# Performance work log

Hardware: AMD Instinct MI355X
Metric: run time of the kernel (lower is better)

Reference implementation:

```python
import jax, jax.numpy as jnp
import numpy as np

B, L, C, K = 32, 8192, 32, 5  # batch, positions, channels(=filters), kernel_size
F = C  # residual add requires filters == input channels
BN_EPS = 1e-3      # keras BatchNormalization default epsilon
LEAKY_ALPHA = 0.3  # keras LeakyReLU default alpha


def setup_inputs() -> dict:
    key = jax.random.key(0)
    ks = jax.random.split(key, 4)
    # RandomUniform(-limit, limit) with limit = sqrt(2*3 / (2*K*F**2))
    limit = float(np.sqrt(2.0 * 3.0 / (2.0 * K * F * F)))
    return {
        "x": jax.random.normal(ks[0], (B, L, C), dtype=jnp.float32),
        # LocallyConnected 1: K unshared kernels [L, C, F], bias [L, F]
        "k1": jax.random.uniform(ks[1], (K, L, C, F), minval=-limit, maxval=limit, dtype=jnp.float32),
        "b1": jnp.zeros((L, F), dtype=jnp.float32),
        "gamma1": jnp.ones((F,), dtype=jnp.float32),
        "beta1": jnp.zeros((F,), dtype=jnp.float32),
        "mean1": jnp.zeros((F,), dtype=jnp.float32),
        "var1": jnp.ones((F,), dtype=jnp.float32),
        # LocallyConnected 2
        "k2": jax.random.uniform(ks[2], (K, L, F, F), minval=-limit, maxval=limit, dtype=jnp.float32),
        "b2": jnp.zeros((L, F), dtype=jnp.float32),
        "gamma2": jnp.ones((F,), dtype=jnp.float32),
        "beta2": jnp.zeros((F,), dtype=jnp.float32),
        "mean2": jnp.zeros((F,), dtype=jnp.float32),
        "var2": jnp.ones((F,), dtype=jnp.float32),
    }


def _locally_connected(x, kernels, bias):
    # x: [B, L, Cin]; kernels: [K, L, Cin, F]; bias: [L, F]
    # Original adds bias once inside the accumulator and once at the end -> 2*bias.
    out = 2.0 * bias
    for i in range(kernels.shape[0]):
        step = (i // 2) * (-1 if (i % 2 == 1) else 1)  # 0, 0, 1, -1, 2, -2, ...
        xs = jnp.roll(x, step, axis=1) if step != 0 else x
        out = out + jnp.einsum('blc,lcf->blf', xs, kernels[i])
    return out


def _bn(x, gamma, beta, mean, var):
    return gamma * (x - mean) * jax.lax.rsqrt(var + BN_EPS) + beta


def _leaky(x):
    return jnp.where(x >= 0, x, LEAKY_ALPHA * x)


def reference(x, k1, b1, gamma1, beta1, mean1, var1,
              k2, b2, gamma2, beta2, mean2, var2):
    h = _locally_connected(x, k1, b1)
    h = _bn(h, gamma1, beta1, mean1, var1)
    h = _leaky(h)
    h = _locally_connected(h, k2, b2)
    h = _bn(h, gamma2, beta2, mean2, var2)
    return _leaky(h + x)
```

## Files before the change

### kernel.cpp

```cpp
#include <hip/hip_runtime.h>

#define LSZ 8192
#define CCH 32
#define NL 8
#define TILE_P (NL + 3)

__global__ __launch_bounds__(512)
void lc_bn_act(const float* __restrict__ xin,
               const float* __restrict__ wgt,
               const float* __restrict__ bias,
               const float* __restrict__ gamma,
               const float* __restrict__ beta,
               const float* __restrict__ mean,
               const float* __restrict__ var,
               const float* __restrict__ xres,
               float* __restrict__ out,
               int resid)
{
    __shared__ __align__(16) float lds[TILE_P * 32 * 32];
    const int tid = threadIdx.x;
    const int l0  = blockIdx.x * NL;

    #pragma unroll
    for (int it = 0; it < (TILE_P * 1024) / 512; ++it) {
        int flat = it * 512 + tid;
        int c  = flat & 31;
        int b  = (flat >> 5) & 31;
        int tp = flat >> 10;
        int p  = (l0 + LSZ - 2 + tp) & (LSZ - 1);
        float v = xin[((size_t)b * LSZ + p) * CCH + c];
        int swz = (((b >> 2) ^ (c & 7)) << 2) | (b & 3);
        lds[tp * 1024 + c * 32 + swz] = v;
    }
    __syncthreads();

    const int wl   = tid >> 6;
    const int lane = tid & 63;
    const int fi   = lane & 7;
    const int bg   = lane >> 3;
    const int l    = l0 + wl;

    float4 acc0 = {0.f,0.f,0.f,0.f};
    float4 acc1 = {0.f,0.f,0.f,0.f};
    float4 acc2 = {0.f,0.f,0.f,0.f};
    float4 acc3 = {0.f,0.f,0.f,0.f};

    const int stepArr[5] = {0, 0, 1, -1, 2};

    #pragma unroll
    for (int i = 0; i < 5; ++i) {
        const int tp = wl + 2 - stepArr[i];
        const float* wp = wgt + (((size_t)i * LSZ + l) << 10) + (fi << 2);
        const float* xp = lds + tp * 1024;
        #pragma unroll 8
        for (int c = 0; c < 32; ++c) {
            float4 w4 = *reinterpret_cast<const float4*>(wp + (c << 5));
            float4 x4 = *reinterpret_cast<const float4*>(xp + (c << 5) + ((bg ^ (c & 7)) << 2));
            acc0.x = fmaf(x4.x, w4.x, acc0.x); acc0.y = fmaf(x4.x, w4.y, acc0.y);
            acc0.z = fmaf(x4.x, w4.z, acc0.z); acc0.w = fmaf(x4.x, w4.w, acc0.w);
            acc1.x = fmaf(x4.y, w4.x, acc1.x); acc1.y = fmaf(x4.y, w4.y, acc1.y);
            acc1.z = fmaf(x4.y, w4.z, acc1.z); acc1.w = fmaf(x4.y, w4.w, acc1.w);
            acc2.x = fmaf(x4.z, w4.x, acc2.x); acc2.y = fmaf(x4.z, w4.y, acc2.y);
            acc2.z = fmaf(x4.z, w4.z, acc2.z); acc2.w = fmaf(x4.z, w4.w, acc2.w);
            acc3.x = fmaf(x4.w, w4.x, acc3.x); acc3.y = fmaf(x4.w, w4.y, acc3.y);
            acc3.z = fmaf(x4.w, w4.z, acc3.z); acc3.w = fmaf(x4.w, w4.w, acc3.w);
        }
    }

    const int f0 = fi << 2;
    float4 g4 = *reinterpret_cast<const float4*>(gamma + f0);
    float4 t4 = *reinterpret_cast<const float4*>(beta  + f0);
    float4 m4 = *reinterpret_cast<const float4*>(mean  + f0);
    float4 v4 = *reinterpret_cast<const float4*>(var   + f0);
    float4 sc, sh;
    sc.x = g4.x * rsqrtf(v4.x + 1e-3f); sh.x = t4.x - m4.x * sc.x;
    sc.y = g4.y * rsqrtf(v4.y + 1e-3f); sh.y = t4.y - m4.y * sc.y;
    sc.z = g4.z * rsqrtf(v4.z + 1e-3f); sh.z = t4.z - m4.z * sc.z;
    sc.w = g4.w * rsqrtf(v4.w + 1e-3f); sh.w = t4.w - m4.w * sc.w;
    float4 bb = *reinterpret_cast<const float4*>(bias + l * 32 + f0);

#define EPILOG(ACC, J)                                                          \
    {                                                                           \
        int b = (bg << 2) + (J);                                                \
        size_t off = ((size_t)b * LSZ + l) * 32 + f0;                           \
        float4 t;                                                               \
        t.x = (ACC.x + 2.f * bb.x) * sc.x + sh.x;                               \
        t.y = (ACC.y + 2.f * bb.y) * sc.y + sh.y;                               \
        t.z = (ACC.z + 2.f * bb.z) * sc.z + sh.z;                               \
        t.w = (ACC.w + 2.f * bb.w) * sc.w + sh.w;                               \
        if (resid) {                                                            \
            float4 r = *reinterpret_cast<const float4*>(xres + off);            \
            t.x += r.x; t.y += r.y; t.z += r.z; t.w += r.w;                     \
        }                                                                       \
        t.x = t.x >= 0.f ? t.x : 0.3f * t.x;                                    \
        t.y = t.y >= 0.f ? t.y : 0.3f * t.y;                                    \
        t.z = t.z >= 0.f ? t.z : 0.3f * t.z;                                    \
        t.w = t.w >= 0.f ? t.w : 0.3f * t.w;                                    \
        *reinterpret_cast<float4*>(out + off) = t;                              \
    }

    EPILOG(acc0, 0)
    EPILOG(acc1, 1)
    EPILOG(acc2, 2)
    EPILOG(acc3, 3)
#undef EPILOG
}

extern "C" void kernel_launch(void* const* d_in, const int* in_sizes, int n_in,
                              void* d_out, int out_size, void* d_ws, size_t ws_size,
                              hipStream_t stream) {
    const float* x   = (const float*)d_in[0];
    const float* k1  = (const float*)d_in[1];
    const float* b1  = (const float*)d_in[2];
    const float* g1  = (const float*)d_in[3];
    const float* be1 = (const float*)d_in[4];
    const float* mn1 = (const float*)d_in[5];
    const float* vr1 = (const float*)d_in[6];
    const float* k2  = (const float*)d_in[7];
    const float* b2  = (const float*)d_in[8];
    const float* g2  = (const float*)d_in[9];
    const float* be2 = (const float*)d_in[10];
    const float* mn2 = (const float*)d_in[11];
    const float* vr2 = (const float*)d_in[12];

    float* h = (float*)d_ws;
    float* o = (float*)d_out;

    dim3 grid(LSZ / NL), block(512);
    hipLaunchKernelGGL(lc_bn_act, grid, block, 0, stream,
                       x, k1, b1, g1, be1, mn1, vr1, x, h, 0);
    hipLaunchKernelGGL(lc_bn_act, grid, block, 0, stream,
                       h, k2, b2, g2, be2, mn2, vr2, x, o, 1);
}
```

Before: 432.8 us.

## Rewrite locally-connected layers with fp16 MFMA and fp16 transposed intermediate

```diff
diff --git a/kernel.cpp b/kernel.cpp
--- a/kernel.cpp
+++ b/kernel.cpp
@@ -1,109 +1,165 @@
 #include <hip/hip_runtime.h>
 
 #define LSZ 8192
-#define CCH 32
-#define NL 8
-#define TILE_P (NL + 3)
+#define STR 40
+#define XROWS 11
 
-__global__ __launch_bounds__(512)
-void lc_bn_act(const float* __restrict__ xin,
-               const float* __restrict__ wgt,
-               const float* __restrict__ bias,
-               const float* __restrict__ gamma,
-               const float* __restrict__ beta,
-               const float* __restrict__ mean,
-               const float* __restrict__ var,
-               const float* __restrict__ xres,
-               float* __restrict__ out,
-               int resid)
+typedef _Float16 f16;
+typedef __attribute__((ext_vector_type(4))) _Float16 f16x4;
+typedef __attribute__((ext_vector_type(8))) _Float16 f16x8;
+typedef __attribute__((ext_vector_type(4))) float f32x4;
+
+__global__ __launch_bounds__(512, 4)
+void lc_mfma(const void* __restrict__ xin_,
+             const float* __restrict__ wgt,
+             const float* __restrict__ bias,
+             const float* __restrict__ gamma, const float* __restrict__ beta,
+             const float* __restrict__ mean,  const float* __restrict__ var,
+             const float* __restrict__ xres,
+             void* __restrict__ out_, int mode)
 {
-    __shared__ __align__(16) float lds[TILE_P * 32 * 32];
-    const int tid = threadIdx.x;
-    const int l0  = blockIdx.x * NL;
+    __shared__ __align__(16) f16 xs[XROWS * 32 * STR];
+    __shared__ __align__(16) f16 ws[8 * 2 * 32 * STR];
 
+    const int tid  = threadIdx.x;
+    const int wl   = tid >> 6;
+    const int lane = tid & 63;
+    const int bid  = blockIdx.x;
+    const int bs   = ((bid & 7) << 7) | (bid >> 3);
+    const int l0   = bs << 3;
+    const int l    = l0 + wl;
+    const int fr   = lane & 15;
+    const int kg   = lane >> 4;
+
+    f16* wsw = ws + wl * (2 * 32 * STR);
+
+    const int cb = lane >> 3;
+    const int fb = lane & 7;
+    const float* wbase = wgt + (size_t)l * 1024 + (size_t)(cb * 4) * 32 + fb * 4;
+    float4 W[2][4];
     #pragma unroll
-    for (int it = 0; it < (TILE_P * 1024) / 512; ++it) {
-        int flat = it * 512 + tid;
-        int c  = flat & 31;
-        int b  = (flat >> 5) & 31;
-        int tp = flat >> 10;
-        int p  = (l0 + LSZ - 2 + tp) & (LSZ - 1);
-        float v = xin[((size_t)b * LSZ + p) * CCH + c];
-        int swz = (((b >> 2) ^ (c & 7)) << 2) | (b & 3);
-        lds[tp * 1024 + c * 32 + swz] = v;
+    for (int r = 0; r < 4; ++r)
+        W[0][r] = *(const float4*)(wbase + (size_t)0 * LSZ * 1024 + r * 32);
+    #pragma unroll
+    for (int r = 0; r < 4; ++r)
+        W[1][r] = *(const float4*)(wbase + (size_t)1 * LSZ * 1024 + r * 32);
+
+    {
+        const int b = lane >> 1, ch = lane & 1;
+        if (mode == 0) {
+            const float* xf = (const float*)xin_;
+            for (int r = wl; r < XROWS; r += 8) {
+                int p = (l0 - 2 + r) & (LSZ - 1);
+                const float* src = xf + ((size_t)b * LSZ + p) * 32 + ch * 16;
+                float4 v0 = *(const float4*)(src + 0);
+                float4 v1 = *(const float4*)(src + 4);
+                float4 v2 = *(const float4*)(src + 8);
+                float4 v3 = *(const float4*)(src + 12);
+                f16x8 h0, h1;
+                h0[0]=(f16)v0.x; h0[1]=(f16)v0.y; h0[2]=(f16)v0.z; h0[3]=(f16)v0.w;
+                h0[4]=(f16)v1.x; h0[5]=(f16)v1.y; h0[6]=(f16)v1.z; h0[7]=(f16)v1.w;
+                h1[0]=(f16)v2.x; h1[1]=(f16)v2.y; h1[2]=(f16)v2.z; h1[3]=(f16)v2.w;
+                h1[4]=(f16)v3.x; h1[5]=(f16)v3.y; h1[6]=(f16)v3.z; h1[7]=(f16)v3.w;
+                *(f16x8*)&xs[(r * 32 + b) * STR + ch * 16 + 0] = h0;
+                *(f16x8*)&xs[(r * 32 + b) * STR + ch * 16 + 8] = h1;
+            }
+        } else {
+            const f16* xh = (const f16*)xin_;
+            for (int r = wl; r < XROWS; r += 8) {
+                int p = (l0 - 2 + r) & (LSZ - 1);
+                const f16* src = xh + (size_t)p * 1024 + b * 32 + ch * 16;
+                f16x8 h0 = *(const f16x8*)(src + 0);
+                f16x8 h1 = *(const f16x8*)(src + 8);
+                *(f16x8*)&xs[(r * 32 + b) * STR + ch * 16 + 0] = h0;
+                *(f16x8*)&xs[(r * 32 + b) * STR + ch * 16 + 8] = h1;
+            }
+        }
     }
     __syncthreads();
 
-    const int wl   = tid >> 6;
-    const int lane = tid & 63;
-    const int fi   = lane & 7;
-    const int bg   = lane >> 3;
-    const int l    = l0 + wl;
+    float scA = gamma[fr]      * rsqrtf(var[fr]      + 1e-3f);
+    float shA = beta[fr]       - mean[fr]      * scA;
+    float scB = gamma[16 + fr] * rsqrtf(var[16 + fr] + 1e-3f);
+    float shB = beta[16 + fr]  - mean[16 + fr] * scB;
+    float bA  = 2.f * bias[l * 32 + fr];
+    float bB  = 2.f * bias[l * 32 + 16 + fr];
 
-    float4 acc0 = {0.f,0.f,0.f,0.f};
-    float4 acc1 = {0.f,0.f,0.f,0.f};
-    float4 acc2 = {0.f,0.f,0.f,0.f};
-    float4 acc3 = {0.f,0.f,0.f,0.f};
+    f32x4 acc00 = {0.f,0.f,0.f,0.f}, acc01 = {0.f,0.f,0.f,0.f};
+    f32x4 acc10 = {0.f,0.f,0.f,0.f}, acc11 = {0.f,0.f,0.f,0.f};
 
-    const int stepArr[5] = {0, 0, 1, -1, 2};
+    const int rof[5] = {2, 2, 1, 3, 0};
 
     #pragma unroll
     for (int i = 0; i < 5; ++i) {
-        const int tp = wl + 2 - stepArr[i];
-        const float* wp = wgt + (((size_t)i * LSZ + l) << 10) + (fi << 2);
-        const float* xp = lds + tp * 1024;
-        #pragma unroll 8
-        for (int c = 0; c < 32; ++c) {
-            float4 w4 = *reinterpret_cast<const float4*>(wp + (c << 5));
-            float4 x4 = *reinterpret_cast<const float4*>(xp + (c << 5) + ((bg ^ (c & 7)) << 2));
-            acc0.x = fmaf(x4.x, w4.x, acc0.x); acc0.y = fmaf(x4.x, w4.y, acc0.y);
-            acc0.z = fmaf(x4.x, w4.z, acc0.z); acc0.w = fmaf(x4.x, w4.w, acc0.w);
-            acc1.x = fmaf(x4.y, w4.x, acc1.x); acc1.y = fmaf(x4.y, w4.y, acc1.y);
-            acc1.z = fmaf(x4.y, w4.z, acc1.z); acc1.w = fmaf(x4.y, w4.w, acc1.w);
-            acc2.x = fmaf(x4.z, w4.x, acc2.x); acc2.y = fmaf(x4.z, w4.y, acc2.y);
-            acc2.z = fmaf(x4.z, w4.z, acc2.z); acc2.w = fmaf(x4.z, w4.w, acc2.w);
-            acc3.x = fmaf(x4.w, w4.x, acc3.x); acc3.y = fmaf(x4.w, w4.y, acc3.y);
-            acc3.z = fmaf(x4.w, w4.z, acc3.z); acc3.w = fmaf(x4.w, w4.w, acc3.w);
+        f16* buf = wsw + (i & 1) * (32 * STR);
+        #pragma unroll
+        for (int q = 0; q < 4; ++q) {
+            f16x4 h;
+            h[0] = (f16)(((const float*)&W[i & 1][0])[q]);
+            h[1] = (f16)(((const float*)&W[i & 1][1])[q]);
+            h[2] = (f16)(((const float*)&W[i & 1][2])[q]);
+            h[3] = (f16)(((const float*)&W[i & 1][3])[q]);
+            *(f16x4*)&buf[(fb * 4 + q) * STR + cb * 4] = h;
+        }
+        if (i < 3) {
+            #pragma unroll
+            for (int r = 0; r < 4; ++r)
+                W[i & 1][r] = *(const float4*)(wbase + (size_t)(i + 2) * LSZ * 1024 + r * 32);
+        }
+        const int rr = wl + rof[i];
+        f16x8 a0 = *(const f16x8*)&xs[(rr * 32 + fr     ) * STR + kg * 8];
+        f16x8 a1 = *(const f16x8*)&xs[(rr * 32 + 16 + fr) * STR + kg * 8];
+        f16x8 b0 = *(const f16x8*)&buf[(fr     ) * STR + kg * 8];
+        f16x8 b1 = *(const f16x8*)&buf[(16 + fr) * STR + kg * 8];
+        acc00 = __builtin_amdgcn_mfma_f32_16x16x32_f16(a0, b0, acc00, 0, 0, 0);
+        acc01 = __builtin_amdgcn_mfma_f32_16x16x32_f16(a0, b1, acc01, 0, 0, 0);
+        acc10 = __builtin_amdgcn_mfma_f32_16x16x32_f16(a1, b0, acc10, 0, 0, 0);
+        acc11 = __builtin_amdgcn_mfma_f32_16x16x32_f16(a1, b1, acc11, 0, 0, 0);
+    }
+
+    if (mode == 0) {
+        f16* rp = wsw;
+        #pragma unroll
+        for (int bt = 0; bt < 2; ++bt) {
+            f32x4 aA = bt ? acc10 : acc00;
+            f32x4 aB = bt ? acc11 : acc01;
+            #pragma unroll
+            for (int j = 0; j < 4; ++j) {
+                int b = bt * 16 + kg * 4 + j;
+                float vA = (aA[j] + bA) * scA + shA;
+                float vB = (aB[j] + bB) * scB + shB;
+                vA = vA >= 0.f ? vA : 0.3f * vA;
+                vB = vB >= 0.f ? vB : 0.3f * vB;
+                rp[b * STR + fr]      = (f16)vA;
+                rp[b * STR + 16 + fr] = (f16)vB;
+            }
+        }
+        const int b2 = lane >> 1, ch = lane & 1;
+        f16x8 r0 = *(const f16x8*)&rp[b2 * STR + ch * 16 + 0];
+        f16x8 r1 = *(const f16x8*)&rp[b2 * STR + ch * 16 + 8];
+        f16* oh = (f16*)out_;
+        *(f16x8*)(oh + (size_t)l * 1024 + b2 * 32 + ch * 16 + 0) = r0;
+        *(f16x8*)(oh + (size_t)l * 1024 + b2 * 32 + ch * 16 + 8) = r1;
+    } else {
+        float* of = (float*)out_;
+        #pragma unroll
+        for (int bt = 0; bt < 2; ++bt) {
+            f32x4 aA = bt ? acc10 : acc00;
+            f32x4 aB = bt ? acc11 : acc01;
+            #pragma unroll
+            for (int j = 0; j < 4; ++j) {
+                int b = bt * 16 + kg * 4 + j;
+                size_t offA = ((size_t)b * LSZ + l) * 32 + fr;
+                size_t offB = offA + 16;
+                float vA = (aA[j] + bA) * scA + shA + xres[offA];
+                float vB = (aB[j] + bB) * scB + shB + xres[offB];
+                vA = vA >= 0.f ? vA : 0.3f * vA;
+                vB = vB >= 0.f ? vB : 0.3f * vB;
+                of[offA] = vA;
+                of[offB] = vB;
+            }
         }
     }
-
-    const int f0 = fi << 2;
-    float4 g4 = *reinterpret_cast<const float4*>(gamma + f0);
-    float4 t4 = *reinterpret_cast<const float4*>(beta  + f0);
-    float4 m4 = *reinterpret_cast<const float4*>(mean  + f0);
-    float4 v4 = *reinterpret_cast<const float4*>(var   + f0);
-    float4 sc, sh;
-    sc.x = g4.x * rsqrtf(v4.x + 1e-3f); sh.x = t4.x - m4.x * sc.x;
-    sc.y = g4.y * rsqrtf(v4.y + 1e-3f); sh.y = t4.y - m4.y * sc.y;
-    sc.z = g4.z * rsqrtf(v4.z + 1e-3f); sh.z = t4.z - m4.z * sc.z;
-    sc.w = g4.w * rsqrtf(v4.w + 1e-3f); sh.w = t4.w - m4.w * sc.w;
-    float4 bb = *reinterpret_cast<const float4*>(bias + l * 32 + f0);
-
-#define EPILOG(ACC, J)                                                          \
-    {                                                                           \
-        int b = (bg << 2) + (J);                                                \
-        size_t off = ((size_t)b * LSZ + l) * 32 + f0;                           \
-        float4 t;                                                               \
-        t.x = (ACC.x + 2.f * bb.x) * sc.x + sh.x;                               \
-        t.y = (ACC.y + 2.f * bb.y) * sc.y + sh.y;                               \
-        t.z = (ACC.z + 2.f * bb.z) * sc.z + sh.z;                               \
-        t.w = (ACC.w + 2.f * bb.w) * sc.w + sh.w;                               \
-        if (resid) {                                                            \
-            float4 r = *reinterpret_cast<const float4*>(xres + off);            \
-            t.x += r.x; t.y += r.y; t.z += r.z; t.w += r.w;                     \
-        }                                                                       \
-        t.x = t.x >= 0.f ? t.x : 0.3f * t.x;                                    \
-        t.y = t.y >= 0.f ? t.y : 0.3f * t.y;                                    \
-        t.z = t.z >= 0.f ? t.z : 0.3f * t.z;                                    \
-        t.w = t.w >= 0.f ? t.w : 0.3f * t.w;                                    \
-        *reinterpret_cast<float4*>(out + off) = t;                              \
-    }
-
-    EPILOG(acc0, 0)
-    EPILOG(acc1, 1)
-    EPILOG(acc2, 2)
-    EPILOG(acc3, 3)
-#undef EPILOG
 }
 
 extern "C" void kernel_launch(void* const* d_in, const int* in_sizes, int n_in,
@@ -123,12 +179,12 @@
     const float* mn2 = (const float*)d_in[11];
     const float* vr2 = (const float*)d_in[12];
 
-    float* h = (float*)d_ws;
-    float* o = (float*)d_out;
+    f16* ht = (f16*)d_ws;
 
-    dim3 grid(LSZ / NL), block(512);
-    hipLaunchKernelGGL(lc_bn_act, grid, block, 0, stream,
-                       x, k1, b1, g1, be1, mn1, vr1, x, h, 0);
-    hipLaunchKernelGGL(lc_bn_act, grid, block, 0, stream,
-                       h, k2, b2, g2, be2, mn2, vr2, x, o, 1);
+    hipLaunchKernelGGL(lc_mfma, dim3(1024), dim3(512), 0, stream,
+                       (const void*)x, k1, b1, g1, be1, mn1, vr1,
+                       (const float*)nullptr, (void*)ht, 0);
+    hipLaunchKernelGGL(lc_mfma, dim3(1024), dim3(512), 0, stream,
+                       (const void*)ht, k2, b2, g2, be2, mn2, vr2,
+                       x, d_out, 1);
 }
```

Result: faster. 391.1 us (-9.6%).
